# Kernel optimization log

Measured on AMD Instinct MI355X. Metric: run time of the kernel, lower is better.

Reference implementation:

```python
import jax, jax.numpy as jnp
import numpy as np

N = 60; L = 4; B = 8192; DIN = 512; DOUT = 256; H = 64; STEPS = 10; DT = 0.1
ZC = float(np.sqrt(3.0) / 2.0)
BOUNDS = jnp.array([0.1, 0.2, 0.4, 0.6, 0.75, ZC, 0.92, 0.97], jnp.float32)
# APL_SYMBOLS order: ['^', '+', 'x', '()', 'div', '-'] ; parity EVEN=+1, ODD=-1
PARITY = jnp.array([1.0, -1.0, 1.0, 1.0, -1.0, -1.0], jnp.float32)
# OPERATOR_WINDOWS per tier t1..t9 -> legal mask over the 6 symbols
LEGAL = jnp.array([
    [0, 0, 0, 1, 1, 1],  # t1: () - div
    [1, 0, 1, 0, 1, 1],  # t2: ^ div - x
    [1, 1, 1, 0, 1, 1],  # t3: x ^ div + -
    [0, 1, 0, 1, 1, 1],  # t4: + - div ()
    [1, 1, 1, 1, 1, 1],  # t5: all
    [0, 1, 0, 1, 1, 1],  # t6: + div () -
    [0, 1, 0, 1, 0, 0],  # t7: + ()
    [0, 1, 1, 1, 0, 0],  # t8: + () x
    [0, 1, 1, 1, 0, 0],  # t9: + () x
], dtype=bool)


def _order(theta):
    # Kuramoto order parameter r = |<e^{i theta}>| per batch row
    return jnp.sqrt(jnp.mean(jnp.cos(theta), -1) ** 2 + jnp.mean(jnp.sin(theta), -1) ** 2)


def setup_inputs() -> dict:
    key = jax.random.key(0)
    ks = jax.random.split(key, 10)
    rn = lambda k, s, sc=1.0: jax.random.normal(k, s, jnp.float32) * sc
    K0 = rn(ks[1], (L, N, N), 0.1)
    K0 = (K0 + jnp.swapaxes(K0, -1, -2)) / 2.0  # symmetric init as in torch
    return {
        'x': rn(ks[0], (B, DIN)),
        'W_enc': rn(ks[2], (DIN, N), 0.04), 'b_enc': jnp.zeros((N,), jnp.float32),
        'K': K0,
        'omega': rn(ks[3], (L, N), 0.1),
        'K_global': jnp.full((L,), 0.5, jnp.float32),
        'apl_K_mod': jnp.full((L, 6), 0.1, jnp.float32),
        'apl_omega_mod': jnp.zeros((L, 6), jnp.float32),
        'W1': rn(ks[4], (L, N + 4, H), 0.1), 'b1': jnp.zeros((L, H), jnp.float32),
        'W2': rn(ks[5], (L, H, H), 0.1), 'b2': jnp.zeros((L, H), jnp.float32),
        'W3': rn(ks[6], (L, H, 6), 0.1), 'b3': jnp.zeros((L, 6), jnp.float32),
        'prior': jnp.ones((L, 6), jnp.float32),
        'noise': rn(ks[7], (L, B, N)),  # frozen randn_like for the 'div' operator branch
        'W_out': rn(ks[8], (2 * N, DOUT), 0.05), 'b_out': jnp.zeros((DOUT,), jnp.float32),
    }


def reference(x, W_enc, b_enc, K, omega, K_global, apl_K_mod, apl_omega_mod,
              W1, b1, W2, b2, W3, b3, prior, noise, W_out, b_out):
    theta = jnp.pi * jnp.tanh(x @ W_enc + b_enc)  # [B, N] initial phases
    for l in range(L):
        coh = _order(theta)                       # [B]
        z = jnp.mean(coh)                         # scalar z-coordinate
        tier = jnp.sum((z >= BOUNDS).astype(jnp.int32))  # 0..8 -> tier t1..t9
        dsneg = jnp.exp(-36.0 * (z - ZC) ** 2)    # compute_delta_s_neg
        bc = lambda v: jnp.broadcast_to(v, (theta.shape[0], 1))
        feats = jnp.concatenate([
            jnp.cos(theta), bc(z), coh[:, None], bc(dsneg),
            bc((tier.astype(jnp.float32) + 1.0) / 9.0)], -1)  # [B, N+4]
        h = jax.nn.gelu(feats @ W1[l] + b1[l], approximate=False)
        h = jax.nn.gelu(h @ W2[l] + b2[l], approximate=False)
        logits = h @ W3[l] + b3[l] + prior[l]     # [B, 6]
        masked = jnp.where(LEGAL[tier], logits, -jnp.inf)
        idx = jnp.argmax(masked[0])               # eval-mode: argmax of row 0
        par = PARITY[idx]
        # apply_apl_operator
        K_eff = K[l] * (1.0 + par * (apl_K_mod[l, idx] * jnp.mean(coh)) * 0.5)
        om_eff = omega[l] + apl_omega_mod[l, idx] * par
        s = jnp.sin(jnp.mean(theta, -1, keepdims=True) - theta)
        coef = jnp.where(idx == 1, 0.1, jnp.where(idx == 5, -0.1, 0.0))  # '+' / '-'
        dmask = jnp.where(idx == 4, 1.0, 0.0)                              # 'div'
        theta = theta + coef * s + dmask * 0.05 * noise[l] * (1.0 - coh[:, None])
        kg = K_global[l]

        def step(th, _):
            diff = th[:, None, :] - th[:, :, None]     # [B,N,N], diff[b,i,j]=th[b,j]-th[b,i]
            csum = jnp.sum(K_eff * jnp.sin(diff), -1)  # [B,N]
            thn = th + DT * (om_eff + kg / N * csum)
            return jnp.arctan2(jnp.sin(thn), jnp.cos(thn)), None

        theta, _ = jax.lax.scan(step, theta, None, length=STEPS)
    coh = _order(theta)
    out = (jnp.concatenate([jnp.cos(theta), jnp.sin(theta)], -1) @ W_out + b_out) * coh[:, None]
    return out
```

## Files before the change

### kernel.cpp

```cpp
#include <hip/hip_runtime.h>
#include <hip/hip_bf16.h>
#include <math.h>

typedef __attribute__((ext_vector_type(8))) short bf16x8v;
typedef __attribute__((ext_vector_type(4))) float f32x4v;
typedef __attribute__((ext_vector_type(4))) unsigned u32x4v;

namespace {

constexpr float PI_F      = 3.14159265358979323846f;
constexpr float TWO_PI_F  = 6.28318530717958647692f;
constexpr float INV_2PI_F = 0.15915494309189533577f;
constexpr float ZC_F      = 0.86602540378443864676f;

__device__ __constant__ float d_BOUNDS[8] = {0.1f, 0.2f, 0.4f, 0.6f, 0.75f,
                                             0.8660254037844386f, 0.92f, 0.97f};
__device__ __constant__ float d_PARITY[6] = {1.f, -1.f, 1.f, 1.f, -1.f, -1.f};
__device__ __constant__ int d_LEGAL[9][6] = {
    {0, 0, 0, 1, 1, 1},
    {1, 0, 1, 0, 1, 1},
    {1, 1, 1, 0, 1, 1},
    {0, 1, 0, 1, 1, 1},
    {1, 1, 1, 1, 1, 1},
    {0, 1, 0, 1, 1, 1},
    {0, 1, 0, 1, 0, 0},
    {0, 1, 1, 1, 0, 0},
    {0, 1, 1, 1, 0, 0}};

__device__ __forceinline__ float wave_sum(float v) {
#pragma unroll
  for (int o = 32; o > 0; o >>= 1) v += __shfl_xor(v, o, 64);
  return v;
}

__device__ __forceinline__ float gelu_exact(float x) {
  return 0.5f * x * (1.0f + erff(x * 0.70710678118654752440f));
}

__device__ __forceinline__ unsigned short f2b(float v) {
  return __builtin_bit_cast(unsigned short, __float2bfloat16(v));
}

__device__ __forceinline__ unsigned pkbf(float a, float b) {
  return ((unsigned)f2b(b) << 16) | (unsigned)f2b(a);
}

}

#define LSTR 36

__global__ __launch_bounds__(256, 2) void enc_mfma(
    const float* __restrict__ x, const float* __restrict__ W_enc,
    const float* __restrict__ b_enc, const float* __restrict__ K,
    const float* __restrict__ W_out, float* __restrict__ theta,
    float* __restrict__ part, unsigned short* __restrict__ Kb,
    unsigned short* __restrict__ Wob) {
  __shared__ float redM[4][16][2];
  const int tid = threadIdx.x;
  const int w = tid >> 6;
  const int lane = tid & 63;
  const int c = lane & 15, g = lane >> 4;
  const int bid = blockIdx.x;
  const int b = bid * 16 + c;
  const bool pad = (w == 3) && (g == 3);
  const int orow = 16 * w + c;
  const bool arow = (orow < 60);
  const f32x4v z4 = {0.f, 0.f, 0.f, 0.f};

  f32x4v em = z4;
  const float* xr = x + (size_t)b * 512 + 8 * g;
  const float* wr0 = W_enc + orow;
#pragma unroll 2
  for (int kt = 0; kt < 16; ++kt) {
    const float4 u0 = *(const float4*)(xr + 32 * kt);
    const float4 u1 = *(const float4*)(xr + 32 * kt + 4);
    u32x4v bx;
    bx[0] = pkbf(u0.x, u0.y); bx[1] = pkbf(u0.z, u0.w);
    bx[2] = pkbf(u1.x, u1.y); bx[3] = pkbf(u1.z, u1.w);
    u32x4v ax;
    if (arow) {
      const float* wp = wr0 + (32 * kt + 8 * g) * 60;
      ax[0] = pkbf(wp[0], wp[60]);
      ax[1] = pkbf(wp[120], wp[180]);
      ax[2] = pkbf(wp[240], wp[300]);
      ax[3] = pkbf(wp[360], wp[420]);
    } else {
      ax[0] = ax[1] = ax[2] = ax[3] = 0u;
    }
    em = __builtin_amdgcn_mfma_f32_16x16x32_bf16(
        __builtin_bit_cast(bf16x8v, ax), __builtin_bit_cast(bf16x8v, bx), em,
        0, 0, 0);
  }
  float th[4], s4[4], c4[4];
  if (!pad) {
    const float4 be = *(const float4*)(b_enc + 16 * w + 4 * g);
    const float bea[4] = {be.x, be.y, be.z, be.w};
#pragma unroll
    for (int r = 0; r < 4; ++r) th[r] = PI_F * tanhf(em[r] + bea[r]);
  } else {
#pragma unroll
    for (int r = 0; r < 4; ++r) th[r] = 0.f;
  }
  float pcc = 0.f, pss = 0.f;
#pragma unroll
  for (int r = 0; r < 4; ++r) {
    s4[r] = __sinf(th[r]);
    c4[r] = __cosf(th[r]);
    pcc += c4[r]; pss += s4[r];
  }
  pcc += __shfl_xor(pcc, 16); pcc += __shfl_xor(pcc, 32);
  pss += __shfl_xor(pss, 16); pss += __shfl_xor(pss, 32);
  redM[w][c][0] = pcc; redM[w][c][1] = pss;
  if (!pad)
    *(float4*)(theta + (size_t)b * 60 + 16 * w + 4 * g) =
        make_float4(th[0], th[1], th[2], th[3]);
  __syncthreads();
  float tc = 0.f, ts = 0.f;
#pragma unroll
  for (int ww = 0; ww < 4; ++ww) { tc += redM[ww][c][0]; ts += redM[ww][c][1]; }
  const float mc = (tc - 4.f) * (1.f / 60.f);
  const float ms = ts * (1.f / 60.f);
  const float ch = sqrtf(mc * mc + ms * ms);
  const float tot = wave_sum(ch) * 0.25f;
  if (tid == 0) part[bid] = tot;

  if (bid < 64) {
    const int t = bid * 256 + tid;
    const int l = t >> 12, rem = t & 4095, i = rem >> 6, k = rem & 63;
    Kb[t] = f2b((i < 60 && k < 60) ? K[l * 3600 + i * 60 + k] : 0.f);
  } else if (bid < 192) {
    const int t = (bid - 64) * 256 + tid;
    const int d = t >> 7, kk = t & 127, prt = kk >> 6, o = kk & 63;
    Wob[t] = f2b((o < 60) ? W_out[(prt * 60 + o) * 256 + d] : 0.f);
  }
}

__global__ __launch_bounds__(256, 2) void kura_mfma(
    float* __restrict__ theta, const float* __restrict__ noiseL,
    const unsigned short* __restrict__ Kb, const unsigned short* __restrict__ Wob,
    const float* __restrict__ omega, const float* __restrict__ Kglob,
    const float* __restrict__ aplK, const float* __restrict__ aplOm,
    const float* __restrict__ W1, const float* __restrict__ b1,
    const float* __restrict__ W2, const float* __restrict__ b2,
    const float* __restrict__ W3, const float* __restrict__ b3,
    const float* __restrict__ prior, const float* __restrict__ b_out,
    float* __restrict__ part, float* __restrict__ out, int l) {
  __shared__ float fe[64], hh[64], lgits[8], scal[4];
  __shared__ float redD[4][64];
  __shared__ float redM[4][16][4];
  __shared__ unsigned sinL[2][16 * LSTR], cosL[2][16 * LSTR];
  __shared__ __align__(16) float trans[16][260];
  const int tid = threadIdx.x;
  const int w = tid >> 6;
  const int lane = tid & 63;
  const int c = lane & 15, g = lane >> 4;
  const int bid = blockIdx.x;
  const int b = bid * 16 + c;
  const bool pad = (w == 3) && (g == 3);
  const f32x4v z4 = {0.f, 0.f, 0.f, 0.f};
  const int o = tid & 63, chx = tid >> 6;

  float z = 0.f;
  int tier = 0;
  if (tid < 64) {
    const float4 p0 = *(const float4*)(part + l * 512 + 8 * lane);
    const float4 p1 = *(const float4*)(part + l * 512 + 8 * lane + 4);
    z = wave_sum(p0.x + p0.y + p0.z + p0.w + p1.x + p1.y + p1.z + p1.w) *
        (1.f / 8192.f);
#pragma unroll
    for (int i = 0; i < 8; ++i) tier += (z >= d_BOUNDS[i]) ? 1 : 0;
    const float dsneg = expf(-36.f * (z - ZC_F) * (z - ZC_F));
    const float th0 = (tid < 60) ? theta[tid] : 0.f;
    const float c00 = __cosf(th0);
    const float pc0 = wave_sum((tid < 60) ? c00 : 0.f) * (1.f / 60.f);
    const float ps0 = wave_sum((tid < 60) ? __sinf(th0) : 0.f) * (1.f / 60.f);
    const float ch0 = sqrtf(pc0 * pc0 + ps0 * ps0);
    fe[tid] = (tid < 60) ? c00
            : (tid == 60) ? z
            : (tid == 61) ? ch0
            : (tid == 62) ? dsneg
                          : (float)(tier + 1) * (1.f / 9.f);
  }
  __syncthreads();
  {
    float a = 0.f;
    const float* Wp = W1 + l * 4096 + (16 * chx) * 64 + o;
#pragma unroll
    for (int kk = 0; kk < 16; ++kk) a = fmaf(fe[16 * chx + kk], Wp[kk * 64], a);
    redD[chx][o] = a;
  }
  __syncthreads();
  if (tid < 64)
    hh[tid] = gelu_exact(redD[0][tid] + redD[1][tid] + redD[2][tid] +
                         redD[3][tid] + b1[l * 64 + tid]);
  __syncthreads();
  {
    float a = 0.f;
    const float* Wp = W2 + l * 4096 + (16 * chx) * 64 + o;
#pragma unroll
    for (int kk = 0; kk < 16; ++kk) a = fmaf(hh[16 * chx + kk], Wp[kk * 64], a);
    redD[chx][o] = a;
  }
  __syncthreads();
  if (tid < 64)
    fe[tid] = gelu_exact(redD[0][tid] + redD[1][tid] + redD[2][tid] +
                         redD[3][tid] + b2[l * 64 + tid]);
  __syncthreads();
  if (tid < 24) {
    const int o3 = tid >> 2, ch3 = tid & 3;
    float a = 0.f;
#pragma unroll
    for (int kk = 0; kk < 16; ++kk)
      a = fmaf(fe[16 * ch3 + kk], W3[l * 384 + (16 * ch3 + kk) * 6 + o3], a);
    redD[ch3][o3] = a;
  }
  __syncthreads();
  if (tid < 6)
    lgits[tid] = redD[0][tid] + redD[1][tid] + redD[2][tid] + redD[3][tid] +
                 b3[l * 6 + tid] + prior[l * 6 + tid];
  __syncthreads();
  if (tid == 0) {
    int idx = 0;
    float best = -INFINITY;
#pragma unroll
    for (int m2 = 0; m2 < 6; ++m2)
      if (d_LEGAL[tier][m2] && lgits[m2] > best) { best = lgits[m2]; idx = m2; }
    const float par = d_PARITY[idx];
    scal[0] = (idx == 1) ? 0.1f : ((idx == 5) ? -0.1f : 0.f);
    scal[1] = (idx == 4) ? 1.f : 0.f;
    scal[2] = (1.f + par * (aplK[l * 6 + idx] * z) * 0.5f) * 0.1f * Kglob[l] *
              (1.f / 60.f);
    scal[3] = aplOm[l * 6 + idx] * par;
  }
  __syncthreads();
  const float coef = scal[0], dmn = scal[1], ktot = scal[2], omadd = scal[3];

  float th[4], s4[4], c4[4], om4[4];
  if (!pad) {
    const float4 t4 = *(const float4*)(theta + (size_t)b * 60 + 16 * w + 4 * g);
    const float4 o4 = *(const float4*)(omega + l * 60 + 16 * w + 4 * g);
    th[0] = t4.x; th[1] = t4.y; th[2] = t4.z; th[3] = t4.w;
    om4[0] = 0.1f * (o4.x + omadd); om4[1] = 0.1f * (o4.y + omadd);
    om4[2] = 0.1f * (o4.z + omadd); om4[3] = 0.1f * (o4.w + omadd);
  } else {
#pragma unroll
    for (int r = 0; r < 4; ++r) { th[r] = 0.f; om4[r] = 0.f; }
  }

  float psum = 0.f, pcc = 0.f, pss = 0.f;
#pragma unroll
  for (int r = 0; r < 4; ++r) {
    psum += th[r];
    pcc += __cosf(th[r]);
    pss += __sinf(th[r]);
  }
  psum += __shfl_xor(psum, 16); psum += __shfl_xor(psum, 32);
  pcc += __shfl_xor(pcc, 16);  pcc += __shfl_xor(pcc, 32);
  pss += __shfl_xor(pss, 16);  pss += __shfl_xor(pss, 32);
  redM[w][c][0] = psum; redM[w][c][1] = pcc; redM[w][c][2] = pss;
  __syncthreads();
  {
    float tsum = 0.f, tc = 0.f, ts = 0.f;
#pragma unroll
    for (int ww = 0; ww < 4; ++ww) {
      tsum += redM[ww][c][0]; tc += redM[ww][c][1]; ts += redM[ww][c][2];
    }
    const float mean = tsum * (1.f / 60.f);
    const float mcp = (tc - 4.f) * (1.f / 60.f);
    const float msp = ts * (1.f / 60.f);
    const float ch_pre = sqrtf(mcp * mcp + msp * msp);
    if (coef != 0.f && !pad) {
#pragma unroll
      for (int r = 0; r < 4; ++r) th[r] += coef * __sinf(mean - th[r]);
    }
    if (dmn != 0.f && !pad) {
      const float f = 0.05f * (1.f - ch_pre);
      const float4 n4 =
          *(const float4*)(noiseL + (size_t)b * 60 + 16 * w + 4 * g);
      th[0] = fmaf(f, n4.x, th[0]); th[1] = fmaf(f, n4.y, th[1]);
      th[2] = fmaf(f, n4.z, th[2]); th[3] = fmaf(f, n4.w, th[3]);
    }
  }
#pragma unroll
  for (int r = 0; r < 4; ++r) { s4[r] = __sinf(th[r]); c4[r] = __cosf(th[r]); }

  const bf16x8v Af0 =
      *(const bf16x8v*)(Kb + l * 4096 + (16 * w + c) * 64 + 8 * g);
  const bf16x8v Af1 =
      *(const bf16x8v*)(Kb + l * 4096 + (16 * w + c) * 64 + 32 + 8 * g);
  const int wr = c * LSTR + 8 * w + 2 * g;
  const int rb = c * LSTR + 4 * g;

  for (int step = 0; step < 10; ++step) {
    const int pb = step & 1;
    *(uint2*)&sinL[pb][wr] = make_uint2(pkbf(s4[0], s4[1]), pkbf(s4[2], s4[3]));
    *(uint2*)&cosL[pb][wr] = make_uint2(pkbf(c4[0], c4[1]), pkbf(c4[2], c4[3]));
    __syncthreads();
    const bf16x8v BS0 = __builtin_bit_cast(bf16x8v, *(const u32x4v*)&sinL[pb][rb]);
    const bf16x8v BS1 = __builtin_bit_cast(bf16x8v, *(const u32x4v*)&sinL[pb][rb + 16]);
    const bf16x8v BC0 = __builtin_bit_cast(bf16x8v, *(const u32x4v*)&cosL[pb][rb]);
    const bf16x8v BC1 = __builtin_bit_cast(bf16x8v, *(const u32x4v*)&cosL[pb][rb + 16]);
    f32x4v t0 = __builtin_amdgcn_mfma_f32_16x16x32_bf16(Af0, BS0, z4, 0, 0, 0);
    const f32x4v P = __builtin_amdgcn_mfma_f32_16x16x32_bf16(Af1, BS1, t0, 0, 0, 0);
    f32x4v t1 = __builtin_amdgcn_mfma_f32_16x16x32_bf16(Af0, BC0, z4, 0, 0, 0);
    const f32x4v Q = __builtin_amdgcn_mfma_f32_16x16x32_bf16(Af1, BC1, t1, 0, 0, 0);
#pragma unroll
    for (int r = 0; r < 4; ++r) {
      const float csum = c4[r] * P[r] - s4[r] * Q[r];
      const float d = fmaf(ktot, csum, om4[r]);
      th[r] += d;
      s4[r] = __sinf(th[r]);
      c4[r] = __cosf(th[r]);
    }
  }

  float pc2 = 0.f, ps2 = 0.f;
#pragma unroll
  for (int r = 0; r < 4; ++r) { pc2 += c4[r]; ps2 += s4[r]; }
  pc2 += __shfl_xor(pc2, 16); pc2 += __shfl_xor(pc2, 32);
  ps2 += __shfl_xor(ps2, 16); ps2 += __shfl_xor(ps2, 32);
  redM[w][c][0] = pc2; redM[w][c][1] = ps2;
  __syncthreads();
  float tc2 = 0.f, ts2 = 0.f;
#pragma unroll
  for (int ww = 0; ww < 4; ++ww) { tc2 += redM[ww][c][0]; ts2 += redM[ww][c][1]; }
  const float mc2 = (tc2 - 4.f) * (1.f / 60.f);
  const float ms2 = ts2 * (1.f / 60.f);
  const float ch = sqrtf(mc2 * mc2 + ms2 * ms2);

  if (l < 3) {
    if (!pad) {
      float wv[4];
#pragma unroll
      for (int r = 0; r < 4; ++r)
        wv[r] = fmaf(-TWO_PI_F, rintf(th[r] * INV_2PI_F), th[r]);
      *(float4*)(theta + (size_t)b * 60 + 16 * w + 4 * g) =
          make_float4(wv[0], wv[1], wv[2], wv[3]);
    }
    const float tot = wave_sum(ch) * 0.25f;
    if (tid == 0) part[(l + 1) * 512 + bid] = tot;
    return;
  }

  *(uint2*)&sinL[0][wr] = make_uint2(pkbf(s4[0], s4[1]), pkbf(s4[2], s4[3]));
  *(uint2*)&cosL[0][wr] = make_uint2(pkbf(c4[0], c4[1]), pkbf(c4[2], c4[3]));
  __syncthreads();
  const bf16x8v BS0 = __builtin_bit_cast(bf16x8v, *(const u32x4v*)&sinL[0][rb]);
  const bf16x8v BS1 = __builtin_bit_cast(bf16x8v, *(const u32x4v*)&sinL[0][rb + 16]);
  const bf16x8v BC0 = __builtin_bit_cast(bf16x8v, *(const u32x4v*)&cosL[0][rb]);
  const bf16x8v BC1 = __builtin_bit_cast(bf16x8v, *(const u32x4v*)&cosL[0][rb + 16]);
#pragma unroll
  for (int i = 0; i < 4; ++i) {
    const int mp = 4 * w + i;
    const unsigned short* ap = Wob + (16 * mp + c) * 128 + 8 * g;
    const bf16x8v A0 = *(const bf16x8v*)(ap);
    const bf16x8v A1 = *(const bf16x8v*)(ap + 32);
    const bf16x8v A2 = *(const bf16x8v*)(ap + 64);
    const bf16x8v A3 = *(const bf16x8v*)(ap + 96);
    f32x4v d = __builtin_amdgcn_mfma_f32_16x16x32_bf16(A0, BC0, z4, 0, 0, 0);
    d = __builtin_amdgcn_mfma_f32_16x16x32_bf16(A1, BC1, d, 0, 0, 0);
    d = __builtin_amdgcn_mfma_f32_16x16x32_bf16(A2, BS0, d, 0, 0, 0);
    d = __builtin_amdgcn_mfma_f32_16x16x32_bf16(A3, BS1, d, 0, 0, 0);
    const float4 bo = *(const float4*)(b_out + 16 * mp + 4 * g);
    *(float4*)(&trans[c][16 * mp + 4 * g]) =
        make_float4((d[0] + bo.x) * ch, (d[1] + bo.y) * ch,
                    (d[2] + bo.z) * ch, (d[3] + bo.w) * ch);
  }
  __syncthreads();
#pragma unroll
  for (int i = 0; i < 4; ++i) {
    const int t = tid + 256 * i;
    const int row = t >> 6, cw = t & 63;
    const float4 v = *(const float4*)(&trans[row][4 * cw]);
    *(float4*)(out + (size_t)(bid * 16 + row) * 256 + 4 * cw) = v;
  }
}

extern "C" void kernel_launch(void* const* d_in, const int* in_sizes, int n_in,
                              void* d_out, int out_size, void* d_ws, size_t ws_size,
                              hipStream_t stream) {
  const float* x     = (const float*)d_in[0];
  const float* W_enc = (const float*)d_in[1];
  const float* b_enc = (const float*)d_in[2];
  const float* K     = (const float*)d_in[3];
  const float* omega = (const float*)d_in[4];
  const float* Kglob = (const float*)d_in[5];
  const float* aplK  = (const float*)d_in[6];
  const float* aplOm = (const float*)d_in[7];
  const float* W1    = (const float*)d_in[8];
  const float* b1    = (const float*)d_in[9];
  const float* W2    = (const float*)d_in[10];
  const float* b2    = (const float*)d_in[11];
  const float* W3    = (const float*)d_in[12];
  const float* b3    = (const float*)d_in[13];
  const float* prior = (const float*)d_in[14];
  const float* noise = (const float*)d_in[15];
  const float* W_out = (const float*)d_in[16];
  const float* b_out = (const float*)d_in[17];

  float* ws    = (float*)d_ws;
  float* theta = ws;
  float* part  = ws + 491520;
  unsigned short* Kb  = (unsigned short*)(ws + 493568);
  unsigned short* Wob = (unsigned short*)(ws + 501760);

  enc_mfma<<<512, 256, 0, stream>>>(x, W_enc, b_enc, K, W_out,
                                    theta, part, Kb, Wob);
  for (int l = 0; l < 4; ++l) {
    kura_mfma<<<512, 256, 0, stream>>>(theta, noise + (size_t)l * 491520,
                                       Kb, Wob, omega, Kglob, aplK, aplOm,
                                       W1, b1, W2, b2, W3, b3, prior, b_out,
                                       part, (float*)d_out, l);
  }
}
```

Before: 57.82 us.

## Stage encoder weights in LDS and run per-layer MLP redundantly per wave

In the encoder kernel, each block now stages W_enc into shared memory as transposed bf16 before the MFMA loop, replacing the strided global loads and per-element conversion done for every k-tile. In the per-layer kernel, every wave computes the small gating MLP and argmax itself, using only wave barriers instead of several block-wide __syncthreads. The theta, omega, noise and K fragment loads are issued early so they overlap with the MLP. The mean and coherence reduction now runs only when the '+', '-' or 'div' operator is selected. The cost is redundant MLP work in four waves, and in the encoder a full W_enc transpose per block plus about 68 KB of LDS, which may reduce occupancy.

```diff
diff --git a/kernel.cpp b/kernel.cpp
--- a/kernel.cpp
+++ b/kernel.cpp
@@ -48,6 +48,7 @@
 }
 
 #define LSTR 36
+#define WSTR 536
 
 __global__ __launch_bounds__(256, 2) void enc_mfma(
     const float* __restrict__ x, const float* __restrict__ W_enc,
@@ -55,6 +56,7 @@
     const float* __restrict__ W_out, float* __restrict__ theta,
     float* __restrict__ part, unsigned short* __restrict__ Kb,
     unsigned short* __restrict__ Wob) {
+  __shared__ unsigned short Wl[64 * WSTR];
   __shared__ float redM[4][16][2];
   const int tid = threadIdx.x;
   const int w = tid >> 6;
@@ -64,32 +66,36 @@
   const int b = bid * 16 + c;
   const bool pad = (w == 3) && (g == 3);
   const int orow = 16 * w + c;
-  const bool arow = (orow < 60);
   const f32x4v z4 = {0.f, 0.f, 0.f, 0.f};
+
+  for (int i = tid; i < 7680; i += 256) {
+    const float4 v = ((const float4*)W_enc)[i];
+    const int base = 4 * i;
+    const float va[4] = {v.x, v.y, v.z, v.w};
+#pragma unroll
+    for (int j = 0; j < 4; ++j) {
+      const int idx = base + j;
+      const int k = idx / 60;
+      const int o = idx - k * 60;
+      Wl[o * WSTR + k] = f2b(va[j]);
+    }
+  }
+  for (int i = tid; i < 4 * WSTR; i += 256) Wl[60 * WSTR + i] = 0;
+  __syncthreads();
 
   f32x4v em = z4;
   const float* xr = x + (size_t)b * 512 + 8 * g;
-  const float* wr0 = W_enc + orow;
-#pragma unroll 2
+  const unsigned short* wl = Wl + orow * WSTR + 8 * g;
+#pragma unroll 4
   for (int kt = 0; kt < 16; ++kt) {
     const float4 u0 = *(const float4*)(xr + 32 * kt);
     const float4 u1 = *(const float4*)(xr + 32 * kt + 4);
     u32x4v bx;
     bx[0] = pkbf(u0.x, u0.y); bx[1] = pkbf(u0.z, u0.w);
     bx[2] = pkbf(u1.x, u1.y); bx[3] = pkbf(u1.z, u1.w);
-    u32x4v ax;
-    if (arow) {
-      const float* wp = wr0 + (32 * kt + 8 * g) * 60;
-      ax[0] = pkbf(wp[0], wp[60]);
-      ax[1] = pkbf(wp[120], wp[180]);
-      ax[2] = pkbf(wp[240], wp[300]);
-      ax[3] = pkbf(wp[360], wp[420]);
-    } else {
-      ax[0] = ax[1] = ax[2] = ax[3] = 0u;
-    }
+    const bf16x8v A = *(const bf16x8v*)(wl + 32 * kt);
     em = __builtin_amdgcn_mfma_f32_16x16x32_bf16(
-        __builtin_bit_cast(bf16x8v, ax), __builtin_bit_cast(bf16x8v, bx), em,
-        0, 0, 0);
+        A, __builtin_bit_cast(bf16x8v, bx), em, 0, 0, 0);
   }
   float th[4], s4[4], c4[4];
   if (!pad) {
@@ -145,8 +151,7 @@
     const float* __restrict__ W3, const float* __restrict__ b3,
     const float* __restrict__ prior, const float* __restrict__ b_out,
     float* __restrict__ part, float* __restrict__ out, int l) {
-  __shared__ float fe[64], hh[64], lgits[8], scal[4];
-  __shared__ float redD[4][64];
+  __shared__ float fe[64], hh[64], f2[64], lg6[8];
   __shared__ float redM[4][16][4];
   __shared__ unsigned sinL[2][16 * LSTR], cosL[2][16 * LSTR];
   __shared__ __align__(16) float trans[16][260];
@@ -158,108 +163,102 @@
   const int b = bid * 16 + c;
   const bool pad = (w == 3) && (g == 3);
   const f32x4v z4 = {0.f, 0.f, 0.f, 0.f};
-  const int o = tid & 63, chx = tid >> 6;
-
-  float z = 0.f;
+
+  float4 t4 = make_float4(0.f, 0.f, 0.f, 0.f);
+  float4 o4 = t4, n4 = t4;
+  if (!pad) {
+    t4 = *(const float4*)(theta + (size_t)b * 60 + 16 * w + 4 * g);
+    o4 = *(const float4*)(omega + l * 60 + 16 * w + 4 * g);
+    n4 = *(const float4*)(noiseL + (size_t)b * 60 + 16 * w + 4 * g);
+  }
+  const bf16x8v Af0 =
+      *(const bf16x8v*)(Kb + l * 4096 + (16 * w + c) * 64 + 8 * g);
+  const bf16x8v Af1 =
+      *(const bf16x8v*)(Kb + l * 4096 + (16 * w + c) * 64 + 32 + 8 * g);
+
+  const float4 p0 = *(const float4*)(part + l * 512 + 8 * lane);
+  const float4 p1 = *(const float4*)(part + l * 512 + 8 * lane + 4);
+  const float z =
+      wave_sum(p0.x + p0.y + p0.z + p0.w + p1.x + p1.y + p1.z + p1.w) *
+      (1.f / 8192.f);
   int tier = 0;
-  if (tid < 64) {
-    const float4 p0 = *(const float4*)(part + l * 512 + 8 * lane);
-    const float4 p1 = *(const float4*)(part + l * 512 + 8 * lane + 4);
-    z = wave_sum(p0.x + p0.y + p0.z + p0.w + p1.x + p1.y + p1.z + p1.w) *
-        (1.f / 8192.f);
-#pragma unroll
-    for (int i = 0; i < 8; ++i) tier += (z >= d_BOUNDS[i]) ? 1 : 0;
-    const float dsneg = expf(-36.f * (z - ZC_F) * (z - ZC_F));
-    const float th0 = (tid < 60) ? theta[tid] : 0.f;
-    const float c00 = __cosf(th0);
-    const float pc0 = wave_sum((tid < 60) ? c00 : 0.f) * (1.f / 60.f);
-    const float ps0 = wave_sum((tid < 60) ? __sinf(th0) : 0.f) * (1.f / 60.f);
-    const float ch0 = sqrtf(pc0 * pc0 + ps0 * ps0);
-    fe[tid] = (tid < 60) ? c00
-            : (tid == 60) ? z
-            : (tid == 61) ? ch0
-            : (tid == 62) ? dsneg
+#pragma unroll
+  for (int i = 0; i < 8; ++i) tier += (z >= d_BOUNDS[i]) ? 1 : 0;
+  const float dsneg = expf(-36.f * (z - ZC_F) * (z - ZC_F));
+  const float th0 = (lane < 60) ? theta[lane] : 0.f;
+  const float c00 = __cosf(th0);
+  const float pc0 = wave_sum((lane < 60) ? c00 : 0.f) * (1.f / 60.f);
+  const float ps0 = wave_sum((lane < 60) ? __sinf(th0) : 0.f) * (1.f / 60.f);
+  const float ch0 = sqrtf(pc0 * pc0 + ps0 * ps0);
+  fe[lane] = (lane < 60) ? c00
+           : (lane == 60) ? z
+           : (lane == 61) ? ch0
+           : (lane == 62) ? dsneg
                           : (float)(tier + 1) * (1.f / 9.f);
-  }
-  __syncthreads();
+  __builtin_amdgcn_wave_barrier();
+  float a0 = b1[l * 64 + lane], a1 = 0.f;
+  const float* W1p = W1 + l * 4096 + lane;
+#pragma unroll 8
+  for (int k = 0; k < 64; k += 2) {
+    a0 = fmaf(fe[k], W1p[k * 64], a0);
+    a1 = fmaf(fe[k + 1], W1p[(k + 1) * 64], a1);
+  }
+  hh[lane] = gelu_exact(a0 + a1);
+  __builtin_amdgcn_wave_barrier();
+  float e0 = b2[l * 64 + lane], e1 = 0.f;
+  const float* W2p = W2 + l * 4096 + lane;
+#pragma unroll 8
+  for (int k = 0; k < 64; k += 2) {
+    e0 = fmaf(hh[k], W2p[k * 64], e0);
+    e1 = fmaf(hh[k + 1], W2p[(k + 1) * 64], e1);
+  }
+  f2[lane] = gelu_exact(e0 + e1);
+  __builtin_amdgcn_wave_barrier();
+  if (lane < 6) {
+    float a3 = b3[l * 6 + lane] + prior[l * 6 + lane];
+    const float* W3p = W3 + l * 384 + lane;
+#pragma unroll 8
+    for (int k = 0; k < 64; ++k) a3 = fmaf(f2[k], W3p[k * 6], a3);
+    lg6[lane] = a3;
+  }
+  __builtin_amdgcn_wave_barrier();
+  int idx = 0;
   {
-    float a = 0.f;
-    const float* Wp = W1 + l * 4096 + (16 * chx) * 64 + o;
-#pragma unroll
-    for (int kk = 0; kk < 16; ++kk) a = fmaf(fe[16 * chx + kk], Wp[kk * 64], a);
-    redD[chx][o] = a;
-  }
-  __syncthreads();
-  if (tid < 64)
-    hh[tid] = gelu_exact(redD[0][tid] + redD[1][tid] + redD[2][tid] +
-                         redD[3][tid] + b1[l * 64 + tid]);
-  __syncthreads();
-  {
-    float a = 0.f;
-    const float* Wp = W2 + l * 4096 + (16 * chx) * 64 + o;
-#pragma unroll
-    for (int kk = 0; kk < 16; ++kk) a = fmaf(hh[16 * chx + kk], Wp[kk * 64], a);
-    redD[chx][o] = a;
-  }
-  __syncthreads();
-  if (tid < 64)
-    fe[tid] = gelu_exact(redD[0][tid] + redD[1][tid] + redD[2][tid] +
-                         redD[3][tid] + b2[l * 64 + tid]);
-  __syncthreads();
-  if (tid < 24) {
-    const int o3 = tid >> 2, ch3 = tid & 3;
-    float a = 0.f;
-#pragma unroll
-    for (int kk = 0; kk < 16; ++kk)
-      a = fmaf(fe[16 * ch3 + kk], W3[l * 384 + (16 * ch3 + kk) * 6 + o3], a);
-    redD[ch3][o3] = a;
-  }
-  __syncthreads();
-  if (tid < 6)
-    lgits[tid] = redD[0][tid] + redD[1][tid] + redD[2][tid] + redD[3][tid] +
-                 b3[l * 6 + tid] + prior[l * 6 + tid];
-  __syncthreads();
-  if (tid == 0) {
-    int idx = 0;
     float best = -INFINITY;
 #pragma unroll
     for (int m2 = 0; m2 < 6; ++m2)
-      if (d_LEGAL[tier][m2] && lgits[m2] > best) { best = lgits[m2]; idx = m2; }
-    const float par = d_PARITY[idx];
-    scal[0] = (idx == 1) ? 0.1f : ((idx == 5) ? -0.1f : 0.f);
-    scal[1] = (idx == 4) ? 1.f : 0.f;
-    scal[2] = (1.f + par * (aplK[l * 6 + idx] * z) * 0.5f) * 0.1f * Kglob[l] *
-              (1.f / 60.f);
-    scal[3] = aplOm[l * 6 + idx] * par;
-  }
-  __syncthreads();
-  const float coef = scal[0], dmn = scal[1], ktot = scal[2], omadd = scal[3];
+      if (d_LEGAL[tier][m2] && lg6[m2] > best) { best = lg6[m2]; idx = m2; }
+  }
+  const float par = d_PARITY[idx];
+  const float coef = (idx == 1) ? 0.1f : ((idx == 5) ? -0.1f : 0.f);
+  const bool dm = (idx == 4);
+  const float ktot =
+      (1.f + par * (aplK[l * 6 + idx] * z) * 0.5f) * 0.1f * Kglob[l] * (1.f / 60.f);
+  const float omadd = aplOm[l * 6 + idx] * par;
 
   float th[4], s4[4], c4[4], om4[4];
+  th[0] = t4.x; th[1] = t4.y; th[2] = t4.z; th[3] = t4.w;
   if (!pad) {
-    const float4 t4 = *(const float4*)(theta + (size_t)b * 60 + 16 * w + 4 * g);
-    const float4 o4 = *(const float4*)(omega + l * 60 + 16 * w + 4 * g);
-    th[0] = t4.x; th[1] = t4.y; th[2] = t4.z; th[3] = t4.w;
     om4[0] = 0.1f * (o4.x + omadd); om4[1] = 0.1f * (o4.y + omadd);
     om4[2] = 0.1f * (o4.z + omadd); om4[3] = 0.1f * (o4.w + omadd);
   } else {
 #pragma unroll
-    for (int r = 0; r < 4; ++r) { th[r] = 0.f; om4[r] = 0.f; }
-  }
-
-  float psum = 0.f, pcc = 0.f, pss = 0.f;
-#pragma unroll
-  for (int r = 0; r < 4; ++r) {
-    psum += th[r];
-    pcc += __cosf(th[r]);
-    pss += __sinf(th[r]);
-  }
-  psum += __shfl_xor(psum, 16); psum += __shfl_xor(psum, 32);
-  pcc += __shfl_xor(pcc, 16);  pcc += __shfl_xor(pcc, 32);
-  pss += __shfl_xor(pss, 16);  pss += __shfl_xor(pss, 32);
-  redM[w][c][0] = psum; redM[w][c][1] = pcc; redM[w][c][2] = pss;
-  __syncthreads();
-  {
+    for (int r = 0; r < 4; ++r) om4[r] = 0.f;
+  }
+
+  if (coef != 0.f || dm) {
+    float psum = 0.f, pcc = 0.f, pss = 0.f;
+#pragma unroll
+    for (int r = 0; r < 4; ++r) {
+      psum += th[r];
+      pcc += __cosf(th[r]);
+      pss += __sinf(th[r]);
+    }
+    psum += __shfl_xor(psum, 16); psum += __shfl_xor(psum, 32);
+    pcc += __shfl_xor(pcc, 16);  pcc += __shfl_xor(pcc, 32);
+    pss += __shfl_xor(pss, 16);  pss += __shfl_xor(pss, 32);
+    redM[w][c][0] = psum; redM[w][c][1] = pcc; redM[w][c][2] = pss;
+    __syncthreads();
     float tsum = 0.f, tc = 0.f, ts = 0.f;
 #pragma unroll
     for (int ww = 0; ww < 4; ++ww) {
@@ -273,10 +272,8 @@
 #pragma unroll
       for (int r = 0; r < 4; ++r) th[r] += coef * __sinf(mean - th[r]);
     }
-    if (dmn != 0.f && !pad) {
+    if (dm && !pad) {
       const float f = 0.05f * (1.f - ch_pre);
-      const float4 n4 =
-          *(const float4*)(noiseL + (size_t)b * 60 + 16 * w + 4 * g);
       th[0] = fmaf(f, n4.x, th[0]); th[1] = fmaf(f, n4.y, th[1]);
       th[2] = fmaf(f, n4.z, th[2]); th[3] = fmaf(f, n4.w, th[3]);
     }
@@ -284,10 +281,6 @@
 #pragma unroll
   for (int r = 0; r < 4; ++r) { s4[r] = __sinf(th[r]); c4[r] = __cosf(th[r]); }
 
-  const bf16x8v Af0 =
-      *(const bf16x8v*)(Kb + l * 4096 + (16 * w + c) * 64 + 8 * g);
-  const bf16x8v Af1 =
-      *(const bf16x8v*)(Kb + l * 4096 + (16 * w + c) * 64 + 32 + 8 * g);
   const int wr = c * LSTR + 8 * w + 2 * g;
   const int rb = c * LSTR + 4 * g;
 
```

Measured after the change: 75.90 us. 31.3% more time.
